# Kernel tuning notes

Hardware: AMD Instinct MI355X
Metric: run time of the kernel (lower is better)

Reference implementation:

```python
import jax, jax.numpy as jnp
import numpy as np

B = 128
NHEAD = 16
D_MODEL = 512
D_IN = 256  # each of f_* and f_*_out; concat -> 512
N_ATOM = 128


def _scopes():
    lens = np.array([96 + (i % 33) for i in range(B)], dtype=np.int64)  # max == 128 == N_ATOM
    starts_a = np.concatenate([[1], 1 + np.cumsum(lens)[:-1]]).astype(np.int64)
    nb = 2 * lens
    starts_b = np.concatenate([[1], 1 + np.cumsum(nb)[:-1]]).astype(np.int64)
    return lens, starts_a, nb, starts_b


def setup_inputs() -> dict:
    key = jax.random.key(0)
    ks = jax.random.split(key, 10)
    lens, starts_a, nb, starts_b = _scopes()
    Na = int(1 + lens.sum())   # 14279 (row 0 is padding)
    Nb = int(1 + nb.sum())     # 28557 (bond 0 is padding)
    f_atoms = jax.random.normal(ks[0], (Na, D_IN), jnp.float32)
    f_bonds = jax.random.normal(ks[1], (Nb, D_IN), jnp.float32)
    f_atoms_out = jax.random.normal(ks[2], (Na, D_IN), jnp.float32)
    f_bonds_out = jax.random.normal(ks[3], (Nb, D_IN), jnp.float32)
    b2a = jax.random.randint(ks[4], (Nb,), 0, 96, jnp.int64 if jax.config.jax_enable_x64 else jnp.int32)
    b2revb = jax.random.randint(ks[5], (Nb,), 0, Nb, b2a.dtype)
    a_scope = jnp.stack([jnp.asarray(starts_a), jnp.asarray(lens)], axis=1)
    b_scope = jnp.stack([jnp.asarray(starts_b), jnp.asarray(nb)], axis=1)
    W_atom = jax.random.normal(ks[6], (2 * D_IN, D_MODEL), jnp.float32) * 0.02
    b_atom = jnp.zeros((D_MODEL,), jnp.float32)
    W_bond = jax.random.normal(ks[7], (2 * D_IN, NHEAD), jnp.float32) * 0.02
    b_bond = jnp.zeros((NHEAD,), jnp.float32)
    return {"f_atoms": f_atoms, "f_bonds": f_bonds, "f_atoms_out": f_atoms_out,
            "f_bonds_out": f_bonds_out, "b2a": b2a, "b2revb": b2revb,
            "a_scope": a_scope, "b_scope": b_scope, "n_atom": N_ATOM,
            "W_atom": W_atom, "b_atom": b_atom, "W_bond": W_bond, "b_bond": b_bond}


def reference(f_atoms, f_bonds, f_atoms_out, f_bonds_out, b2a, b2revb,
              a_scope, b_scope, n_atom, W_atom, b_atom, W_bond, b_bond):
    Bsz = a_scope.shape[0]
    # atom embedding: concat + linear, drop padding row 0, pad per-molecule -> [n_atom, B, d]
    atoms = jnp.concatenate([f_atoms, f_atoms_out], axis=1) @ W_atom + b_atom  # [Na, d]
    starts_a, lens_a = a_scope[:, 0], a_scope[:, 1]
    pos = jnp.arange(n_atom)
    valid = pos[None, :] < lens_a[:, None]                       # [B, n_atom]
    gidx = jnp.where(valid, starts_a[:, None] + pos[None, :], 0)  # safe gather idx
    atoms_pad = jnp.where(valid[..., None], atoms[gidx], 0.0)     # [B, n_atom, d]
    atoms_emb = atoms_pad.transpose(1, 0, 2)                      # [n_atom, B, d] (batch_first=False)
    # bond embedding -> scatter into dense pairwise matrix
    bonds = jnp.concatenate([f_bonds, f_bonds_out], axis=1) @ W_bond + b_bond  # [Nb, nhead]
    Nb = bonds.shape[0]
    starts_b = b_scope[:, 0]
    mol = jnp.searchsorted(starts_b, jnp.arange(Nb), side='right') - 1  # molecule id per bond (-1 for pad bond 0)
    offset = jnp.maximum(mol, 0) * (n_atom * n_atom)
    idx = b2a + b2a[b2revb] * n_atom + offset                     # flat index into [B*n_atom*n_atom]
    flat = jnp.zeros((Bsz * n_atom * n_atom, bonds.shape[1]), bonds.dtype).at[idx].set(bonds)
    apairs = flat.reshape(Bsz, n_atom, n_atom, -1)                # [B, n_atom, n_atom, nhead]
    padding_mask = ~valid                                         # [B, n_atom], True = pad
    apairs = jnp.where(padding_mask[:, None, :, None], -jnp.inf, apairs)
    apairs = apairs.transpose(0, 3, 1, 2)                         # [B, nhead, n_atom, n_atom]
    return atoms_emb, apairs, padding_mask
```

## Files before the change

### kernel.cpp

```cpp
#include <hip/hip_runtime.h>
#include <math.h>

#define NEG_BIG (-1e30f)

typedef __attribute__((ext_vector_type(8))) short short8;
typedef __attribute__((ext_vector_type(8))) _Float16 half8;
typedef __attribute__((ext_vector_type(4))) float floatx4;

__device__ __forceinline__ unsigned short f2bf(float x) {
    unsigned u = __float_as_uint(x);
    unsigned r = (u + 0x7fffu + ((u >> 16) & 1u)) >> 16;
    return (unsigned short)r;
}

__device__ __forceinline__ short f2h(float x) {
    _Float16 h = (_Float16)x;
    return __builtin_bit_cast(short, h);
}
__device__ __forceinline__ float h2f(short s) {
    return (float)__builtin_bit_cast(_Float16, s);
}

__global__ void k_init(int* __restrict__ w, int n) {
    int t = blockIdx.x * 256 + threadIdx.x;
    if (t < n) w[t] = -1;
}

__global__ void k_prepWa(const float* __restrict__ W, short* __restrict__ H,
                         short* __restrict__ L) {
    int t = blockIdx.x * 256 + threadIdx.x;
    int n = t >> 9, k = t & 511;
    float x = W[(size_t)k * 512 + n];
    short h = f2h(x);
    float r = (x - h2f(h)) * 2048.0f;
    H[t] = h;
    L[t] = f2h(r);
}

__global__ void k_prepWb(const float* __restrict__ Wb, short* __restrict__ Wbt) {
    int t = blockIdx.x * 256 + threadIdx.x;
    int h = t >> 9, k = t & 511;
    Wbt[t] = (short)f2bf(Wb[(size_t)k * 16 + h]);
}

__global__ __launch_bounds__(256, 2) void k_atoms_mfma(
    const float* __restrict__ fA, const float* __restrict__ fAo,
    const int* __restrict__ a_scope,
    const short* __restrict__ WH, const short* __restrict__ WL,
    const float* __restrict__ bias, float* __restrict__ out, int Bmol)
{
    __shared__ short A_s[2][128 * 40];
    __shared__ short B_s[2][128 * 40];
    __shared__ int rs[128];

    const int tid = threadIdx.x;
    const int n0 = blockIdx.x * 128;
    const int mol = blockIdx.y;

    if (tid < 128) {
        int len = a_scope[2 * mol + 1];
        rs[tid] = (tid < len) ? (a_scope[2 * mol] + tid) : -1;
    }
    const int wid = tid >> 6, lane = tid & 63;
    const int wm = (wid >> 1) * 64, wn = (wid & 1) * 64;
    const int quad = lane >> 4, l16 = lane & 15;

    floatx4 acc1[4][4], acc2[4][4];
#pragma unroll
    for (int i = 0; i < 4; i++)
#pragma unroll
        for (int j = 0; j < 4; j++) {
            acc1[i][j] = (floatx4){0.f, 0.f, 0.f, 0.f};
            acc2[i][j] = (floatx4){0.f, 0.f, 0.f, 0.f};
        }

    const int ar = tid >> 1;
    const int ak = (tid & 1) * 16;
    __syncthreads();
    const int asrc = rs[ar];

    for (int k0 = 0; k0 < 512; k0 += 32) {
        float x[16];
        if (asrc >= 0) {
            int kg = k0 + ak;
            const float* p = (kg < 256) ? (fA + (size_t)asrc * 256 + kg)
                                        : (fAo + (size_t)asrc * 256 + (kg - 256));
#pragma unroll
            for (int i = 0; i < 4; i++) {
                float4 v = ((const float4*)p)[i];
                x[i * 4 + 0] = v.x; x[i * 4 + 1] = v.y;
                x[i * 4 + 2] = v.z; x[i * 4 + 3] = v.w;
            }
        } else {
#pragma unroll
            for (int i = 0; i < 16; i++) x[i] = 0.f;
        }
        size_t goff = (size_t)(n0 + ar) * 512 + k0 + ak;
        short8 bh0 = *(const short8*)(WH + goff);
        short8 bh1 = *(const short8*)(WH + goff + 8);
        short8 bl0 = *(const short8*)(WL + goff);
        short8 bl1 = *(const short8*)(WL + goff + 8);

        short8 ah0, ah1, al0, al1;
#pragma unroll
        for (int i = 0; i < 8; i++) {
            short h = f2h(x[i]);
            float r = (x[i] - h2f(h)) * 2048.0f;
            ah0[i] = h; al0[i] = f2h(r);
        }
#pragma unroll
        for (int i = 0; i < 8; i++) {
            float xx = x[8 + i];
            short h = f2h(xx);
            float r = (xx - h2f(h)) * 2048.0f;
            ah1[i] = h; al1[i] = f2h(r);
        }

        __syncthreads();
        const int abase = ar * 40 + ak;
        *(short8*)&A_s[0][abase] = ah0; *(short8*)&A_s[0][abase + 8] = ah1;
        *(short8*)&A_s[1][abase] = al0; *(short8*)&A_s[1][abase + 8] = al1;
        *(short8*)&B_s[0][abase] = bh0; *(short8*)&B_s[0][abase + 8] = bh1;
        *(short8*)&B_s[1][abase] = bl0; *(short8*)&B_s[1][abase + 8] = bl1;
        __syncthreads();

        half8 afh[4], afl[4];
#pragma unroll
        for (int ti = 0; ti < 4; ti++) {
            int off = (wm + ti * 16 + l16) * 40 + quad * 8;
            afh[ti] = *(const half8*)&A_s[0][off];
            afl[ti] = *(const half8*)&A_s[1][off];
        }
#pragma unroll
        for (int tj = 0; tj < 4; tj++) {
            int off = (wn + tj * 16 + l16) * 40 + quad * 8;
            half8 bh = *(const half8*)&B_s[0][off];
            half8 bl = *(const half8*)&B_s[1][off];
#pragma unroll
            for (int ti = 0; ti < 4; ti++) {
                acc1[ti][tj] = __builtin_amdgcn_mfma_f32_16x16x32_f16(afh[ti], bh, acc1[ti][tj], 0, 0, 0);
                acc2[ti][tj] = __builtin_amdgcn_mfma_f32_16x16x32_f16(afh[ti], bl, acc2[ti][tj], 0, 0, 0);
                acc2[ti][tj] = __builtin_amdgcn_mfma_f32_16x16x32_f16(afl[ti], bh, acc2[ti][tj], 0, 0, 0);
            }
        }
    }

#pragma unroll
    for (int tj = 0; tj < 4; tj++) {
        int n = n0 + wn + tj * 16 + l16;
        float bv = bias[n];
#pragma unroll
        for (int ti = 0; ti < 4; ti++) {
#pragma unroll
            for (int r = 0; r < 4; r++) {
                int pos = wm + ti * 16 + quad * 4 + r;
                bool valid = rs[pos] >= 0;
                float v = valid ? (acc1[ti][tj][r] + 4.8828125e-4f * acc2[ti][tj][r] + bv) : 0.f;
                out[((size_t)pos * Bmol + mol) * 512 + n] = v;
            }
        }
    }
}

__global__ __launch_bounds__(256) void k_bonds_mfma(
    const float* __restrict__ fB, const float* __restrict__ fBo,
    const short* __restrict__ Wbt, const float* __restrict__ bb_,
    float* __restrict__ bonds, int Nb)
{
    __shared__ short feat[64 * 136];
    __shared__ short wb[16 * 512];

    const int tid = threadIdx.x;
    const int j0 = blockIdx.x * 64;

    for (int c = tid; c < 1024; c += 256) {
        int h = c >> 6, cc = c & 63;
        short8 v = *(const short8*)(Wbt + h * 512 + cc * 8);
        *(short8*)&wb[h * 512 + (((cc + h) & 63) * 8)] = v;
    }

    const int wid = tid >> 6, lane = tid & 63;
    const int quad = lane >> 4, l16 = lane & 15;
    floatx4 acc = (floatx4){0.f, 0.f, 0.f, 0.f};

    const int fr = tid >> 2;
    const int fs = (tid & 3) * 32;
    const int j = j0 + fr;

    for (int k0 = 0; k0 < 512; k0 += 128) {
        float x[32];
        if (j < Nb) {
            const float* p = (k0 < 256) ? (fB + (size_t)j * 256 + k0 + fs)
                                        : (fBo + (size_t)j * 256 + (k0 - 256) + fs);
#pragma unroll
            for (int i = 0; i < 8; i++) {
                float4 v = ((const float4*)p)[i];
                x[i * 4 + 0] = v.x; x[i * 4 + 1] = v.y;
                x[i * 4 + 2] = v.z; x[i * 4 + 3] = v.w;
            }
        } else {
#pragma unroll
            for (int i = 0; i < 32; i++) x[i] = 0.f;
        }
        __syncthreads();
#pragma unroll
        for (int c = 0; c < 4; c++) {
            short8 s;
#pragma unroll
            for (int i = 0; i < 8; i++) s[i] = (short)f2bf(x[c * 8 + i]);
            *(short8*)&feat[fr * 136 + fs + c * 8] = s;
        }
        __syncthreads();
#pragma unroll
        for (int kk = 0; kk < 4; kk++) {
            short8 a = *(const short8*)&feat[(wid * 16 + l16) * 136 + kk * 32 + quad * 8];
            int kchunk = (k0 + kk * 32 + quad * 8) >> 3;
            short8 b = *(const short8*)&wb[l16 * 512 + (((kchunk + l16) & 63) * 8)];
            acc = __builtin_amdgcn_mfma_f32_16x16x32_bf16(a, b, acc, 0, 0, 0);
        }
    }
    float bv = bb_[l16];
#pragma unroll
    for (int r = 0; r < 4; r++) {
        int jj = j0 + wid * 16 + quad * 4 + r;
        if (jj < Nb) bonds[(size_t)jj * 16 + l16] = acc[r] + bv;
    }
}

__global__ void k_scatter(const int* __restrict__ b2a, const int* __restrict__ b2revb,
                          const int* __restrict__ b_scope, int* __restrict__ winner,
                          int Nb, int Bmol)
{
    __shared__ int sb[128];
    int tid = threadIdx.x;
    if (tid < Bmol) sb[tid] = b_scope[2 * tid];
    __syncthreads();
    int j = blockIdx.x * 256 + tid;
    if (j >= Nb) return;
    int lo = 0, hi = Bmol;
    while (lo < hi) { int mid = (lo + hi) >> 1; if (sb[mid] <= j) lo = mid + 1; else hi = mid; }
    int mol = lo - 1; if (mol < 0) mol = 0;
    int p2 = b2a[j];
    int p1 = b2a[b2revb[j]];
    atomicMax(&winner[mol * 16384 + p1 * 128 + p2], j);
}

__global__ __launch_bounds__(256) void k_apairs(
    const int* __restrict__ winner, const float* __restrict__ bonds,
    const int* __restrict__ a_scope, float* __restrict__ out, int Bmol)
{
    int t = blockIdx.x * 256 + threadIdx.x;
    int b = t >> 12;
    int p1 = (t >> 5) & 127;
    int p2q = t & 31;
    int len = a_scope[2 * b + 1];
    const int4 w = ((const int4*)winner)[t];

    int wi0 = w.x, wi1 = w.y, wi2 = w.z, wi3 = w.w;
    float rows[4][16];
#pragma unroll
    for (int c = 0; c < 16; c++) {
        rows[0][c] = 0.f; rows[1][c] = 0.f; rows[2][c] = 0.f; rows[3][c] = 0.f;
    }
    if (wi0 >= 0) {
        const float4* p = (const float4*)(bonds + (size_t)wi0 * 16);
#pragma unroll
        for (int c = 0; c < 4; c++) {
            float4 v = p[c];
            rows[0][4*c+0] = v.x; rows[0][4*c+1] = v.y; rows[0][4*c+2] = v.z; rows[0][4*c+3] = v.w;
        }
    }
    if (wi1 >= 0) {
        const float4* p = (const float4*)(bonds + (size_t)wi1 * 16);
#pragma unroll
        for (int c = 0; c < 4; c++) {
            float4 v = p[c];
            rows[1][4*c+0] = v.x; rows[1][4*c+1] = v.y; rows[1][4*c+2] = v.z; rows[1][4*c+3] = v.w;
        }
    }
    if (wi2 >= 0) {
        const float4* p = (const float4*)(bonds + (size_t)wi2 * 16);
#pragma unroll
        for (int c = 0; c < 4; c++) {
            float4 v = p[c];
            rows[2][4*c+0] = v.x; rows[2][4*c+1] = v.y; rows[2][4*c+2] = v.z; rows[2][4*c+3] = v.w;
        }
    }
    if (wi3 >= 0) {
        const float4* p = (const float4*)(bonds + (size_t)wi3 * 16);
#pragma unroll
        for (int c = 0; c < 4; c++) {
            float4 v = p[c];
            rows[3][4*c+0] = v.x; rows[3][4*c+1] = v.y; rows[3][4*c+2] = v.z; rows[3][4*c+3] = v.w;
        }
    }

    bool iv0 = (p2q * 4 + 0 >= len);
    bool iv1 = (p2q * 4 + 1 >= len);
    bool iv2 = (p2q * 4 + 2 >= len);
    bool iv3 = (p2q * 4 + 3 >= len);
    float* ob = out + ((size_t)b * 16 * 128 + p1) * 128 + p2q * 4;
#pragma unroll
    for (int h = 0; h < 16; h++) {
        float4 v;
        v.x = iv0 ? NEG_BIG : rows[0][h];
        v.y = iv1 ? NEG_BIG : rows[1][h];
        v.z = iv2 ? NEG_BIG : rows[2][h];
        v.w = iv3 ? NEG_BIG : rows[3][h];
        *(float4*)(ob + (size_t)h * 16384) = v;
    }
}

__global__ void k_mask(const int* __restrict__ a_scope, float* __restrict__ out, int Bmol) {
    int t = blockIdx.x * 256 + threadIdx.x;
    if (t >= Bmol * 128) return;
    int b = t >> 7, p = t & 127;
    out[t] = (p >= a_scope[2 * b + 1]) ? 1.0f : 0.0f;
}

extern "C" void kernel_launch(void* const* d_in, const int* in_sizes, int n_in,
                              void* d_out, int out_size, void* d_ws, size_t ws_size,
                              hipStream_t stream)
{
    const float* f_atoms     = (const float*)d_in[0];
    const float* f_bonds     = (const float*)d_in[1];
    const float* f_atoms_out = (const float*)d_in[2];
    const float* f_bonds_out = (const float*)d_in[3];
    const int*   b2a         = (const int*)d_in[4];
    const int*   b2revb      = (const int*)d_in[5];
    const int*   a_scope     = (const int*)d_in[6];
    const int*   b_scope     = (const int*)d_in[7];
    const float* W_atom      = (const float*)d_in[9];
    const float* b_atom      = (const float*)d_in[10];
    const float* W_bond      = (const float*)d_in[11];
    const float* b_bond      = (const float*)d_in[12];

    const int Bmol = in_sizes[6] / 2;
    const int Nb   = in_sizes[4];

    char* ws = (char*)d_ws;
    size_t off = 0;
    float* bonds_ws = (float*)(ws + off); off += ((size_t)Nb * 16 * 4 + 255) & ~(size_t)255;
    int*   winner   = (int*)(ws + off);   off += (size_t)Bmol * 16384 * 4;
    short* WH       = (short*)(ws + off); off += 512 * 512 * 2;
    short* WL       = (short*)(ws + off); off += 512 * 512 * 2;
    short* Wbt      = (short*)(ws + off); off += 16 * 512 * 2;

    float* out_emb  = (float*)d_out;
    float* out_ap   = out_emb + (size_t)128 * Bmol * 512;
    float* out_mask = out_ap + (size_t)Bmol * 16 * 128 * 128;

    const int ncell = Bmol * 16384;
    hipLaunchKernelGGL(k_prepWa, dim3(1024), dim3(256), 0, stream, W_atom, WH, WL);
    hipLaunchKernelGGL(k_prepWb, dim3(32), dim3(256), 0, stream, W_bond, Wbt);
    hipLaunchKernelGGL(k_init, dim3((ncell + 255) / 256), dim3(256), 0, stream, winner, ncell);
    hipLaunchKernelGGL(k_atoms_mfma, dim3(4, Bmol), dim3(256), 0, stream,
                       f_atoms, f_atoms_out, a_scope, WH, WL, b_atom, out_emb, Bmol);
    hipLaunchKernelGGL(k_bonds_mfma, dim3((Nb + 63) / 64), dim3(256), 0, stream,
                       f_bonds, f_bonds_out, Wbt, b_bond, bonds_ws, Nb);
    hipLaunchKernelGGL(k_scatter, dim3((Nb + 255) / 256), dim3(256), 0, stream,
                       b2a, b2revb, b_scope, winner, Nb, Bmol);
    hipLaunchKernelGGL(k_apairs, dim3(Bmol * 4096 / 256), dim3(256), 0, stream,
                       winner, bonds_ws, a_scope, out_ap, Bmol);
    hipLaunchKernelGGL(k_mask, dim3((Bmol * 128 + 255) / 256), dim3(256), 0, stream,
                       a_scope, out_mask, Bmol);
}
```

Before: 300.9 us.

## Fuse launches into prep/main/commit and replace dense apairs gather with fill plus sparse commit

Merges the eight kernel launches into three. A prep kernel handles the weight conversion, winner init and mask. A main kernel runs atoms GEMM, bonds GEMM, the dense -inf/0 fill of apairs and the atomic scatter in disjoint block ranges. A commit kernel then writes only the winning bond rows into the pre-filled apairs instead of gathering for every cell. The goal is to cut launch gaps and the per-cell winner reads and gathers, and to let the memory-bound fill overlap the GEMMs. The cost is shared-memory sizing for the largest role, and the commit kernel's scattered strided 4-byte stores.

```diff
diff --git a/kernel.cpp b/kernel.cpp
--- a/kernel.cpp
+++ b/kernel.cpp
@@ -12,7 +12,6 @@
     unsigned r = (u + 0x7fffu + ((u >> 16) & 1u)) >> 16;
     return (unsigned short)r;
 }
-
 __device__ __forceinline__ short f2h(float x) {
     _Float16 h = (_Float16)x;
     return __builtin_bit_cast(short, h);
@@ -21,41 +20,62 @@
     return (float)__builtin_bit_cast(_Float16, s);
 }
 
-__global__ void k_init(int* __restrict__ w, int n) {
-    int t = blockIdx.x * 256 + threadIdx.x;
-    if (t < n) w[t] = -1;
-}
-
-__global__ void k_prepWa(const float* __restrict__ W, short* __restrict__ H,
-                         short* __restrict__ L) {
-    int t = blockIdx.x * 256 + threadIdx.x;
-    int n = t >> 9, k = t & 511;
-    float x = W[(size_t)k * 512 + n];
-    short h = f2h(x);
-    float r = (x - h2f(h)) * 2048.0f;
-    H[t] = h;
-    L[t] = f2h(r);
-}
-
-__global__ void k_prepWb(const float* __restrict__ Wb, short* __restrict__ Wbt) {
-    int t = blockIdx.x * 256 + threadIdx.x;
-    int h = t >> 9, k = t & 511;
-    Wbt[t] = (short)f2bf(Wb[(size_t)k * 16 + h]);
-}
-
-__global__ __launch_bounds__(256, 2) void k_atoms_mfma(
+__global__ __launch_bounds__(256) void k_prep(
+    const float* __restrict__ W, short* __restrict__ H, short* __restrict__ L,
+    const float* __restrict__ Wb, short* __restrict__ Wbt,
+    int* __restrict__ winner,
+    const int* __restrict__ a_scope, float* __restrict__ mask_out, int Bmol)
+{
+    int bid = blockIdx.x;
+    int tid = threadIdx.x;
+    if (bid < 1024) {
+        int t = bid * 256 + tid;
+        int n = t >> 9, k = t & 511;
+        float x = W[(size_t)k * 512 + n];
+        short h = f2h(x);
+        float r = (x - h2f(h)) * 2048.0f;
+        H[t] = h;
+        L[t] = f2h(r);
+        return;
+    }
+    bid -= 1024;
+    if (bid < 32) {
+        int t = bid * 256 + tid;
+        int h = t >> 9, k = t & 511;
+        Wbt[t] = (short)f2bf(Wb[(size_t)k * 16 + h]);
+        return;
+    }
+    bid -= 32;
+    if (bid < Bmol * 16) {
+        int t = bid * 256 + tid;
+        ((int4*)winner)[t] = make_int4(-1, -1, -1, -1);
+        return;
+    }
+    bid -= Bmol * 16;
+    {
+        int t = bid * 256 + tid;
+        if (t < Bmol * 128) {
+            int b = t >> 7, p = t & 127;
+            mask_out[t] = (p >= a_scope[2 * b + 1]) ? 1.0f : 0.0f;
+        }
+    }
+}
+
+
+__device__ __forceinline__ void atoms_body(
+    int abid, char* smem,
     const float* __restrict__ fA, const float* __restrict__ fAo,
     const int* __restrict__ a_scope,
     const short* __restrict__ WH, const short* __restrict__ WL,
     const float* __restrict__ bias, float* __restrict__ out, int Bmol)
 {
-    __shared__ short A_s[2][128 * 40];
-    __shared__ short B_s[2][128 * 40];
-    __shared__ int rs[128];
+    short* A_s = (short*)smem;
+    short* B_s = (short*)(smem + 20480);
+    int*   rs  = (int*)(smem + 40960);
 
     const int tid = threadIdx.x;
-    const int n0 = blockIdx.x * 128;
-    const int mol = blockIdx.y;
+    const int n0 = (abid & 3) * 128;
+    const int mol = abid >> 2;
 
     if (tid < 128) {
         int len = a_scope[2 * mol + 1];
@@ -118,24 +138,24 @@
 
         __syncthreads();
         const int abase = ar * 40 + ak;
-        *(short8*)&A_s[0][abase] = ah0; *(short8*)&A_s[0][abase + 8] = ah1;
-        *(short8*)&A_s[1][abase] = al0; *(short8*)&A_s[1][abase + 8] = al1;
-        *(short8*)&B_s[0][abase] = bh0; *(short8*)&B_s[0][abase + 8] = bh1;
-        *(short8*)&B_s[1][abase] = bl0; *(short8*)&B_s[1][abase + 8] = bl1;
+        *(short8*)&A_s[abase] = ah0;          *(short8*)&A_s[abase + 8] = ah1;
+        *(short8*)&A_s[5120 + abase] = al0;   *(short8*)&A_s[5120 + abase + 8] = al1;
+        *(short8*)&B_s[abase] = bh0;          *(short8*)&B_s[abase + 8] = bh1;
+        *(short8*)&B_s[5120 + abase] = bl0;   *(short8*)&B_s[5120 + abase + 8] = bl1;
         __syncthreads();
 
         half8 afh[4], afl[4];
 #pragma unroll
         for (int ti = 0; ti < 4; ti++) {
             int off = (wm + ti * 16 + l16) * 40 + quad * 8;
-            afh[ti] = *(const half8*)&A_s[0][off];
-            afl[ti] = *(const half8*)&A_s[1][off];
+            afh[ti] = *(const half8*)&A_s[off];
+            afl[ti] = *(const half8*)&A_s[5120 + off];
         }
 #pragma unroll
         for (int tj = 0; tj < 4; tj++) {
             int off = (wn + tj * 16 + l16) * 40 + quad * 8;
-            half8 bh = *(const half8*)&B_s[0][off];
-            half8 bl = *(const half8*)&B_s[1][off];
+            half8 bh = *(const half8*)&B_s[off];
+            half8 bl = *(const half8*)&B_s[5120 + off];
 #pragma unroll
             for (int ti = 0; ti < 4; ti++) {
                 acc1[ti][tj] = __builtin_amdgcn_mfma_f32_16x16x32_f16(afh[ti], bh, acc1[ti][tj], 0, 0, 0);
@@ -162,16 +182,17 @@
     }
 }
 
-__global__ __launch_bounds__(256) void k_bonds_mfma(
+__device__ __forceinline__ void bonds_body(
+    int bbid, char* smem,
     const float* __restrict__ fB, const float* __restrict__ fBo,
     const short* __restrict__ Wbt, const float* __restrict__ bb_,
     float* __restrict__ bonds, int Nb)
 {
-    __shared__ short feat[64 * 136];
-    __shared__ short wb[16 * 512];
+    short* feat = (short*)smem;
+    short* wb   = (short*)(smem + 17408);
 
     const int tid = threadIdx.x;
-    const int j0 = blockIdx.x * 64;
+    const int j0 = bbid * 64;
 
     for (int c = tid; c < 1024; c += 256) {
         int h = c >> 6, cc = c & 63;
@@ -227,9 +248,83 @@
     }
 }
 
-__global__ void k_scatter(const int* __restrict__ b2a, const int* __restrict__ b2revb,
-                          const int* __restrict__ b_scope, int* __restrict__ winner,
-                          int Nb, int Bmol)
+__device__ __forceinline__ void fill_body(
+    int fbid, const int* __restrict__ a_scope, float* __restrict__ out_ap)
+{
+    int f = fbid * 256 + threadIdx.x;
+    int r = f >> 3;
+    int b = r >> 11;
+    int p2b = (f & 7) * 16;
+    int len = a_scope[2 * b + 1];
+    float4* dst = (float4*)(out_ap + (size_t)f * 16);
+#pragma unroll
+    for (int c = 0; c < 4; c++) {
+        float4 v;
+        v.x = (p2b + c * 4 + 0 >= len) ? NEG_BIG : 0.f;
+        v.y = (p2b + c * 4 + 1 >= len) ? NEG_BIG : 0.f;
+        v.z = (p2b + c * 4 + 2 >= len) ? NEG_BIG : 0.f;
+        v.w = (p2b + c * 4 + 3 >= len) ? NEG_BIG : 0.f;
+        dst[c] = v;
+    }
+}
+
+__device__ __forceinline__ void scatter_body(
+    int sbid, char* smem,
+    const int* __restrict__ b2a, const int* __restrict__ b2revb,
+    const int* __restrict__ b_scope, int* __restrict__ winner,
+    int Nb, int Bmol)
+{
+    int* sb = (int*)smem;
+    int tid = threadIdx.x;
+    if (tid < Bmol) sb[tid] = b_scope[2 * tid];
+    __syncthreads();
+    int j = sbid * 256 + tid;
+    if (j >= Nb) return;
+    int lo = 0, hi = Bmol;
+    while (lo < hi) { int mid = (lo + hi) >> 1; if (sb[mid] <= j) lo = mid + 1; else hi = mid; }
+    int mol = lo - 1; if (mol < 0) mol = 0;
+    int p2 = b2a[j];
+    int p1 = b2a[b2revb[j]];
+    atomicMax(&winner[mol * 16384 + p1 * 128 + p2], j);
+}
+
+__global__ __launch_bounds__(256, 2) void k_main(
+    const float* __restrict__ fA, const float* __restrict__ fAo,
+    const float* __restrict__ fB, const float* __restrict__ fBo,
+    const int* __restrict__ b2a, const int* __restrict__ b2revb,
+    const int* __restrict__ a_scope, const int* __restrict__ b_scope,
+    const short* __restrict__ WH, const short* __restrict__ WL,
+    const short* __restrict__ Wbt,
+    const float* __restrict__ b_atom, const float* __restrict__ b_bond,
+    float* __restrict__ out_emb, float* __restrict__ out_ap,
+    float* __restrict__ bonds_ws, int* __restrict__ winner,
+    int Bmol, int Nb, int nAtomsB, int nBondsB, int nFillB)
+{
+    __shared__ char smem[41472];
+    int bid = blockIdx.x;
+    if (bid < nAtomsB) {
+        atoms_body(bid, smem, fA, fAo, a_scope, WH, WL, b_atom, out_emb, Bmol);
+        return;
+    }
+    bid -= nAtomsB;
+    if (bid < nBondsB) {
+        bonds_body(bid, smem, fB, fBo, Wbt, b_bond, bonds_ws, Nb);
+        return;
+    }
+    bid -= nBondsB;
+    if (bid < nFillB) {
+        fill_body(bid, a_scope, out_ap);
+        return;
+    }
+    bid -= nFillB;
+    scatter_body(bid, smem, b2a, b2revb, b_scope, winner, Nb, Bmol);
+}
+
+__global__ __launch_bounds__(256) void k_commit(
+    const int* __restrict__ b2a, const int* __restrict__ b2revb,
+    const int* __restrict__ b_scope, const int* __restrict__ a_scope,
+    const int* __restrict__ winner, const float* __restrict__ bonds,
+    float* __restrict__ out_ap, int Nb, int Bmol)
 {
     __shared__ int sb[128];
     int tid = threadIdx.x;
@@ -242,80 +337,16 @@
     int mol = lo - 1; if (mol < 0) mol = 0;
     int p2 = b2a[j];
     int p1 = b2a[b2revb[j]];
-    atomicMax(&winner[mol * 16384 + p1 * 128 + p2], j);
-}
-
-__global__ __launch_bounds__(256) void k_apairs(
-    const int* __restrict__ winner, const float* __restrict__ bonds,
-    const int* __restrict__ a_scope, float* __restrict__ out, int Bmol)
-{
-    int t = blockIdx.x * 256 + threadIdx.x;
-    int b = t >> 12;
-    int p1 = (t >> 5) & 127;
-    int p2q = t & 31;
-    int len = a_scope[2 * b + 1];
-    const int4 w = ((const int4*)winner)[t];
-
-    int wi0 = w.x, wi1 = w.y, wi2 = w.z, wi3 = w.w;
-    float rows[4][16];
-#pragma unroll
-    for (int c = 0; c < 16; c++) {
-        rows[0][c] = 0.f; rows[1][c] = 0.f; rows[2][c] = 0.f; rows[3][c] = 0.f;
-    }
-    if (wi0 >= 0) {
-        const float4* p = (const float4*)(bonds + (size_t)wi0 * 16);
-#pragma unroll
-        for (int c = 0; c < 4; c++) {
-            float4 v = p[c];
-            rows[0][4*c+0] = v.x; rows[0][4*c+1] = v.y; rows[0][4*c+2] = v.z; rows[0][4*c+3] = v.w;
-        }
-    }
-    if (wi1 >= 0) {
-        const float4* p = (const float4*)(bonds + (size_t)wi1 * 16);
-#pragma unroll
-        for (int c = 0; c < 4; c++) {
-            float4 v = p[c];
-            rows[1][4*c+0] = v.x; rows[1][4*c+1] = v.y; rows[1][4*c+2] = v.z; rows[1][4*c+3] = v.w;
-        }
-    }
-    if (wi2 >= 0) {
-        const float4* p = (const float4*)(bonds + (size_t)wi2 * 16);
-#pragma unroll
-        for (int c = 0; c < 4; c++) {
-            float4 v = p[c];
-            rows[2][4*c+0] = v.x; rows[2][4*c+1] = v.y; rows[2][4*c+2] = v.z; rows[2][4*c+3] = v.w;
-        }
-    }
-    if (wi3 >= 0) {
-        const float4* p = (const float4*)(bonds + (size_t)wi3 * 16);
-#pragma unroll
-        for (int c = 0; c < 4; c++) {
-            float4 v = p[c];
-            rows[3][4*c+0] = v.x; rows[3][4*c+1] = v.y; rows[3][4*c+2] = v.z; rows[3][4*c+3] = v.w;
-        }
-    }
-
-    bool iv0 = (p2q * 4 + 0 >= len);
-    bool iv1 = (p2q * 4 + 1 >= len);
-    bool iv2 = (p2q * 4 + 2 >= len);
-    bool iv3 = (p2q * 4 + 3 >= len);
-    float* ob = out + ((size_t)b * 16 * 128 + p1) * 128 + p2q * 4;
-#pragma unroll
-    for (int h = 0; h < 16; h++) {
-        float4 v;
-        v.x = iv0 ? NEG_BIG : rows[0][h];
-        v.y = iv1 ? NEG_BIG : rows[1][h];
-        v.z = iv2 ? NEG_BIG : rows[2][h];
-        v.w = iv3 ? NEG_BIG : rows[3][h];
-        *(float4*)(ob + (size_t)h * 16384) = v;
-    }
-}
-
-__global__ void k_mask(const int* __restrict__ a_scope, float* __restrict__ out, int Bmol) {
-    int t = blockIdx.x * 256 + threadIdx.x;
-    if (t >= Bmol * 128) return;
-    int b = t >> 7, p = t & 127;
-    out[t] = (p >= a_scope[2 * b + 1]) ? 1.0f : 0.0f;
+    int cell = mol * 16384 + p1 * 128 + p2;
+    if (winner[cell] != j) return;
+    if (p2 >= a_scope[2 * mol + 1]) return;
+    const float4* src = (const float4*)(bonds + (size_t)j * 16);
+    float4 v0 = src[0], v1 = src[1], v2 = src[2], v3 = src[3];
+    float vals[16] = {v0.x, v0.y, v0.z, v0.w, v1.x, v1.y, v1.z, v1.w,
+                      v2.x, v2.y, v2.z, v2.w, v3.x, v3.y, v3.z, v3.w};
+    float* dst = out_ap + ((size_t)mol * 16 * 128 + p1) * 128 + p2;
+#pragma unroll
+    for (int h = 0; h < 16; h++) dst[(size_t)h * 16384] = vals[h];
 }
 
 extern "C" void kernel_launch(void* const* d_in, const int* in_sizes, int n_in,
@@ -350,18 +381,21 @@
     float* out_ap   = out_emb + (size_t)128 * Bmol * 512;
     float* out_mask = out_ap + (size_t)Bmol * 16 * 128 * 128;
 
-    const int ncell = Bmol * 16384;
-    hipLaunchKernelGGL(k_prepWa, dim3(1024), dim3(256), 0, stream, W_atom, WH, WL);
-    hipLaunchKernelGGL(k_prepWb, dim3(32), dim3(256), 0, stream, W_bond, Wbt);
-    hipLaunchKernelGGL(k_init, dim3((ncell + 255) / 256), dim3(256), 0, stream, winner, ncell);
-    hipLaunchKernelGGL(k_atoms_mfma, dim3(4, Bmol), dim3(256), 0, stream,
-                       f_atoms, f_atoms_out, a_scope, WH, WL, b_atom, out_emb, Bmol);
-    hipLaunchKernelGGL(k_bonds_mfma, dim3((Nb + 63) / 64), dim3(256), 0, stream,
-                       f_bonds, f_bonds_out, Wbt, b_bond, bonds_ws, Nb);
-    hipLaunchKernelGGL(k_scatter, dim3((Nb + 255) / 256), dim3(256), 0, stream,
-                       b2a, b2revb, b_scope, winner, Nb, Bmol);
-    hipLaunchKernelGGL(k_apairs, dim3(Bmol * 4096 / 256), dim3(256), 0, stream,
-                       winner, bonds_ws, a_scope, out_ap, Bmol);
-    hipLaunchKernelGGL(k_mask, dim3((Bmol * 128 + 255) / 256), dim3(256), 0, stream,
-                       a_scope, out_mask, Bmol);
-}
+    const int prepB = 1024 + 32 + Bmol * 16 + (Bmol * 128 + 255) / 256;
+    hipLaunchKernelGGL(k_prep, dim3(prepB), dim3(256), 0, stream,
+                       W_atom, WH, WL, W_bond, Wbt, winner, a_scope, out_mask, Bmol);
+
+    const int nAtomsB = 4 * Bmol;
+    const int nBondsB = (Nb + 63) / 64;
+    const int nFillB  = Bmol * 64;
+    const int nScatB  = (Nb + 255) / 256;
+    hipLaunchKernelGGL(k_main, dim3(nAtomsB + nBondsB + nFillB + nScatB), dim3(256), 0, stream,
+                       f_atoms, f_atoms_out, f_bonds, f_bonds_out,
+                       b2a, b2revb, a_scope, b_scope,
+                       WH, WL, Wbt, b_atom, b_bond,
+                       out_emb, out_ap, bonds_ws, winner,
+                       Bmol, Nb, nAtomsB, nBondsB, nFillB);
+
+    hipLaunchKernelGGL(k_commit, dim3(nScatB), dim3(256), 0, stream,
+                       b2a, b2revb, b_scope, a_scope, winner, bonds_ws, out_ap, Nb, Bmol);
+}
```

Result: slower. 332.6 us (+10.5%).
